# Performance work log

Measured on AMD Instinct MI355X. Metric: run time of the kernel, lower is better.

The kernel has to match this reference:

```python
import jax, jax.numpy as jnp
import numpy as np

TAU = 2.0        # spikingjelly LIFNode default tau
VTH = 1.0        # v_threshold
ALPHA = 2.0      # ATan surrogate alpha
NUM_HEADS = 8
N_WIN = 8
TOPK = 4


@jax.custom_vjp
def atan_heaviside(x):
    # spike = H(v - v_th), with ATan surrogate gradient
    return (x >= 0.0).astype(x.dtype)

def _ah_fwd(x):
    return atan_heaviside(x), x

def _ah_bwd(x, g):
    half_pi_alpha = np.float32(np.pi / 2.0 * ALPHA)
    return (g * (ALPHA / 2.0) / (1.0 + (half_pi_alpha * x) ** 2),)

atan_heaviside.defvjp(_ah_fwd, _ah_bwd)


def lif(x):
    """Multi-step LIF over leading time dim. decay_input=True, v_reset=0, detach_reset."""
    def step(v, xt):
        v = v + (xt - v) / TAU                      # charge
        s = atan_heaviside(v - VTH)                 # fire
        v = v * (1.0 - jax.lax.stop_gradient(s))    # hard reset (detached)
        return v, s
    _, spikes = jax.lax.scan(step, jnp.zeros_like(x[0]), x)
    return spikes


def setup_inputs() -> dict:
    key = jax.random.key(0)
    k1, k2, k3, k4, k5 = jax.random.split(key, 5)
    T, B, L, C = 4, 4, 1024, 256
    x = jax.random.normal(k1, (T, B, L, C), dtype=jnp.float32)
    w_qkv = jax.random.normal(k2, (C, 3 * C), dtype=jnp.float32) * (C ** -0.5)
    b_qkv = jax.random.normal(k3, (3 * C,), dtype=jnp.float32) * 0.02
    w_proj = jax.random.normal(k4, (C, C), dtype=jnp.float32) * (C ** -0.5)
    b_proj = jax.random.normal(k5, (C,), dtype=jnp.float32) * 0.02
    return {"x": x, "w_qkv": w_qkv, "b_qkv": b_qkv, "w_proj": w_proj, "b_proj": b_proj}


def reference(x, w_qkv, b_qkv, w_proj, b_proj):
    T, B, L, C = x.shape
    hd = C // NUM_HEADS
    win = L // N_WIN
    scale = hd ** -0.5

    # --- region-level routing (on raw input summed over time) ---
    xs = x.sum(axis=0).reshape(B, N_WIN, win, C)
    region = xs.sum(axis=2)                                  # [B, n_win, C]
    attn_r = jnp.einsum('bnc,bmc->bnm', region, region) * (C ** -0.5)
    _, idx = jax.lax.top_k(attn_r, TOPK)                     # [B, n_win, topk] int32

    # --- qkv + LIF spiking ---
    qkv = x @ w_qkv + b_qkv                                  # [T,B,L,3C]
    q, k, v = jnp.split(qkv, 3, axis=-1)
    q, k, v = lif(q), lif(k), lif(v)
    q = q.reshape(T, B, N_WIN, win, NUM_HEADS, hd)
    k = k.reshape(T, B, N_WIN, win, NUM_HEADS, hd)
    v = v.reshape(T, B, N_WIN, win, NUM_HEADS, hd)

    # --- gather routed KV windows (vectorized; topk-major concat like torch.cat) ---
    b_idx = jnp.arange(B)[:, None, None]                     # [B,1,1]
    k_g = k[:, b_idx, idx].reshape(T, B, N_WIN, TOPK * win, NUM_HEADS, hd)
    v_g = v[:, b_idx, idx].reshape(T, B, N_WIN, TOPK * win, NUM_HEADS, hd)

    # --- windowed attention over gathered keys ---
    attn = jnp.einsum('tbnqhd,tbnkhd->tbnhqk', q, k_g) * scale
    attn = jax.nn.softmax(attn, axis=-1)
    out = jnp.einsum('tbnhqk,tbnkhd->tbnqhd', attn, v_g).reshape(T, B, L, C)

    out = lif(out @ w_proj + b_proj)
    return out
```

## Files before the change

### kernel.cpp

```cpp
#include <hip/hip_runtime.h>
#include <cstdint>
#include <cstddef>

#define TT 4
#define BB 4
#define LL 1024
#define CC 256
#define HH 8
#define HD 32
#define NWIN 8
#define WIN 128
#define TOPKN 4
#define C3 768

__global__ __launch_bounds__(64) void region_kernel(const float* __restrict__ x,
                                                    float* __restrict__ region) {
    int bn = blockIdx.x;
    int b = bn >> 3, n = bn & 7;
    int c = blockIdx.y * 64 + threadIdx.x;
    float tot = 0.0f;
    for (int r = 0; r < WIN; ++r) {
        int l = n * WIN + r;
        float s = 0.0f;
        for (int t = 0; t < TT; ++t) {
            s += x[(((size_t)t * BB + b) * LL + l) * CC + c];
        }
        tot += s;
    }
    region[(size_t)bn * CC + c] = tot;
}

__global__ __launch_bounds__(64) void route_kernel(const float* __restrict__ region,
                                                   int* __restrict__ idx) {
    int b = blockIdx.x;
    __shared__ float reg[NWIN][CC];
    __shared__ float attn_r[NWIN][NWIN];
    int tid = threadIdx.x;
    for (int e = tid; e < NWIN * CC; e += 64)
        reg[e >> 8][e & 255] = region[(size_t)b * NWIN * CC + e];
    __syncthreads();
    int n = tid >> 3, m = tid & 7;
    float s = 0.0f;
    for (int c = 0; c < CC; ++c) s += reg[n][c] * reg[m][c];
    attn_r[n][m] = s * 0.0625f;
    __syncthreads();
    if (tid < NWIN) {
        float vals[NWIN];
        for (int m2 = 0; m2 < NWIN; ++m2) vals[m2] = attn_r[tid][m2];
        for (int kk = 0; kk < TOPKN; ++kk) {
            int bi = 0; float bv = vals[0];
            for (int m2 = 1; m2 < NWIN; ++m2) {
                if (vals[m2] > bv) { bv = vals[m2]; bi = m2; }
            }
            idx[(b * NWIN + tid) * TOPKN + kk] = bi;
            vals[bi] = -INFINITY;
        }
    }
}

__global__ __launch_bounds__(256, 3) void gemm_bias128(const float* __restrict__ A,
                                                       const float* __restrict__ W,
                                                       const float* __restrict__ bias,
                                                       float* __restrict__ C,
                                                       int M, int N, int K) {
    const int BM = 128, BN = 128, BK = 16, TM = 8;
    __shared__ float As[BK][BM + 4];
    __shared__ float Bs[BK][136];
    int tid = threadIdx.x;
    int tx = tid & 15, ty = tid >> 4;
    int bm = blockIdx.x * BM, bn = blockIdx.y * BN;
    float acc[TM][8] = {};
    for (int k0 = 0; k0 < K; k0 += BK) {
#pragma unroll
        for (int it = 0; it < 2; ++it) {
            int i = it * 256 + tid;
            int row = i >> 2, kc = (i & 3) * 4;
            float4 v = *(const float4*)(A + (size_t)(bm + row) * K + k0 + kc);
            As[kc + 0][row] = v.x; As[kc + 1][row] = v.y;
            As[kc + 2][row] = v.z; As[kc + 3][row] = v.w;
        }
#pragma unroll
        for (int it = 0; it < 2; ++it) {
            int i = it * 256 + tid;
            int kr = i >> 5, nc = (i & 31) * 4;
            float4 v = *(const float4*)(W + (size_t)(k0 + kr) * N + bn + nc);
            *(float4*)&Bs[kr][nc] = v;
        }
        __syncthreads();
#pragma unroll
        for (int kk = 0; kk < BK; ++kk) {
            float a[TM], bb[8];
            const float4* ap = (const float4*)&As[kk][ty * TM];
            float4 a0 = ap[0], a1 = ap[1];
            a[0]=a0.x; a[1]=a0.y; a[2]=a0.z; a[3]=a0.w;
            a[4]=a1.x; a[5]=a1.y; a[6]=a1.z; a[7]=a1.w;
            float4 b0 = *(const float4*)&Bs[kk][tx * 4];
            float4 b1 = *(const float4*)&Bs[kk][64 + tx * 4];
            bb[0]=b0.x; bb[1]=b0.y; bb[2]=b0.z; bb[3]=b0.w;
            bb[4]=b1.x; bb[5]=b1.y; bb[6]=b1.z; bb[7]=b1.w;
#pragma unroll
            for (int i = 0; i < TM; ++i)
#pragma unroll
                for (int j = 0; j < 8; ++j)
                    acc[i][j] = fmaf(a[i], bb[j], acc[i][j]);
        }
        __syncthreads();
    }
#pragma unroll
    for (int i = 0; i < TM; ++i) {
        int row = bm + ty * TM + i;
        int col0 = bn + tx * 4;
        int col1 = bn + 64 + tx * 4;
        float4 o0 = make_float4(acc[i][0] + bias[col0 + 0], acc[i][1] + bias[col0 + 1],
                                acc[i][2] + bias[col0 + 2], acc[i][3] + bias[col0 + 3]);
        float4 o1 = make_float4(acc[i][4] + bias[col1 + 0], acc[i][5] + bias[col1 + 1],
                                acc[i][6] + bias[col1 + 2], acc[i][7] + bias[col1 + 3]);
        *(float4*)&C[(size_t)row * N + col0] = o0;
        *(float4*)&C[(size_t)row * N + col1] = o1;
    }
}

__global__ __launch_bounds__(256, 4) void gemm_bias64(const float* __restrict__ A,
                                                      const float* __restrict__ W,
                                                      const float* __restrict__ bias,
                                                      float* __restrict__ C,
                                                      int M, int N, int K) {
    const int BM = 64, BN = 64, BK = 16;
    __shared__ float As[BK][BM + 4];
    __shared__ float Bs[BK][72];
    int tid = threadIdx.x;
    int tx = tid & 15, ty = tid >> 4;
    int bm = blockIdx.x * BM, bn = blockIdx.y * BN;
    float acc[4][4] = {};
    for (int k0 = 0; k0 < K; k0 += BK) {
        {
            int row = tid >> 2, kc = (tid & 3) * 4;
            float4 v = *(const float4*)(A + (size_t)(bm + row) * K + k0 + kc);
            As[kc + 0][row] = v.x; As[kc + 1][row] = v.y;
            As[kc + 2][row] = v.z; As[kc + 3][row] = v.w;
        }
        {
            int kr = tid >> 4, nc = (tid & 15) * 4;
            float4 v = *(const float4*)(W + (size_t)(k0 + kr) * N + bn + nc);
            *(float4*)&Bs[kr][nc] = v;
        }
        __syncthreads();
#pragma unroll
        for (int kk = 0; kk < BK; ++kk) {
            float4 av = *(const float4*)&As[kk][ty * 4];
            float4 bv = *(const float4*)&Bs[kk][tx * 4];
            float a[4] = {av.x, av.y, av.z, av.w};
            float bb[4] = {bv.x, bv.y, bv.z, bv.w};
#pragma unroll
            for (int i = 0; i < 4; ++i)
#pragma unroll
                for (int j = 0; j < 4; ++j)
                    acc[i][j] = fmaf(a[i], bb[j], acc[i][j]);
        }
        __syncthreads();
    }
#pragma unroll
    for (int i = 0; i < 4; ++i) {
        int row = bm + ty * 4 + i;
        int col = bn + tx * 4;
        float4 o = make_float4(acc[i][0] + bias[col + 0], acc[i][1] + bias[col + 1],
                               acc[i][2] + bias[col + 2], acc[i][3] + bias[col + 3]);
        *(float4*)&C[(size_t)row * N + col] = o;
    }
}

__global__ __launch_bounds__(256) void lif_kernel(const float* src, float* dst, size_t stride) {
    size_t i = ((size_t)blockIdx.x * blockDim.x + threadIdx.x) * 4;
    float v[4] = {0.f, 0.f, 0.f, 0.f};
    for (int t = 0; t < TT; ++t) {
        float4 xv4 = *(const float4*)(src + (size_t)t * stride + i);
        float xv[4] = {xv4.x, xv4.y, xv4.z, xv4.w};
        float sp[4];
#pragma unroll
        for (int j = 0; j < 4; ++j) {
            v[j] = v[j] + (xv[j] - v[j]) * 0.5f;
            bool fire = (v[j] >= 1.0f);
            sp[j] = fire ? 1.0f : 0.0f;
            v[j] = fire ? 0.0f : v[j];
        }
        *(float4*)(dst + (size_t)t * stride + i) = make_float4(sp[0], sp[1], sp[2], sp[3]);
    }
}

__global__ __launch_bounds__(192) void lif_pack_kernel(float* __restrict__ qkv,
                                                       uint32_t* __restrict__ pk) {
    int row = blockIdx.x;
    int tid = threadIdx.x;
    int c = tid * 4;
    int wid = tid >> 6;
    int lane = tid & 63;
    const size_t stride = (size_t)BB * LL * C3;
    float* base = qkv + (size_t)row * C3 + c;

    float v[4] = {0.f, 0.f, 0.f, 0.f};
    for (int t = 0; t < TT; ++t) {
        float4 xv4 = *(const float4*)(base + (size_t)t * stride);
        float xv[4] = {xv4.x, xv4.y, xv4.z, xv4.w};
        bool fire[4];
        float sp[4];
#pragma unroll
        for (int j = 0; j < 4; ++j) {
            v[j] = v[j] + (xv[j] - v[j]) * 0.5f;
            fire[j] = (v[j] >= 1.0f);
            sp[j] = fire[j] ? 1.0f : 0.0f;
            v[j] = fire[j] ? 0.0f : v[j];
        }
        if (c >= 512)
            *(float4*)(base + (size_t)t * stride) = make_float4(sp[0], sp[1], sp[2], sp[3]);
        unsigned long long B0 = __ballot(fire[0]);
        unsigned long long B1 = __ballot(fire[1]);
        unsigned long long B2 = __ballot(fire[2]);
        unsigned long long B3 = __ballot(fire[3]);
        if (lane < 8 && wid < 2) {
            uint32_t word = ((uint32_t)(B0 >> (8 * lane)) & 0xFFu)
                          | (((uint32_t)(B1 >> (8 * lane)) & 0xFFu) << 8)
                          | (((uint32_t)(B2 >> (8 * lane)) & 0xFFu) << 16)
                          | (((uint32_t)(B3 >> (8 * lane)) & 0xFFu) << 24);
            pk[((size_t)t * BB * LL + row) * 16 + wid * 8 + lane] = word;
        }
    }
}

__global__ __launch_bounds__(256, 4) void attn_pv(const float* __restrict__ spk,
                                                  const uint32_t* __restrict__ pk,
                                                  const int* __restrict__ idxws,
                                                  float* __restrict__ out) {
    int bid = blockIdx.x;
    int h = bid & 1, hp = (bid >> 1) & 3, n = (bid >> 3) & 7, b = (bid >> 6) & 3, t = bid >> 8;
    __shared__ __align__(16) float Vlds[2][64][32];
    __shared__ float ptab[33][WIN];
    __shared__ __align__(16) uint32_t kbs[4 * WIN];
    int tid = threadIdx.x;
    int qg = tid & 63, dh = tid >> 6;
    int lbase = (t * BB + b) * LL;

    const int* ip = idxws + (b * NWIN + n) * TOPKN;
    int s0r = ip[0], s1r = ip[1], s2r = ip[2], s3r = ip[3];

#pragma unroll 2
    for (int e = tid; e < 512; e += 256) {
        int w = e >> 7;
        int sw = (w == 0) ? s0r : (w == 1) ? s1r : (w == 2) ? s2r : s3r;
        int row = sw * WIN + (e & 127);
        kbs[e] = pk[(size_t)(lbase + row) * 16 + 8 + hp * 2 + h];
    }
    uint32_t qw0 = pk[(size_t)(lbase + n * WIN + qg) * 16 + hp * 2 + h];
    uint32_t qw1 = pk[(size_t)(lbase + n * WIN + qg + 64) * 16 + hp * 2 + h];

    const float* vsrc = spk + (size_t)lbase * C3 + 512 + hp * 64 + h * 32
                        + (size_t)(tid >> 3) * C3 + (tid & 7) * 4;
    int wvoff = (tid >> 6) * 1024;

#define STAGE_HALF(hw_)                                                              \
    do {                                                                             \
        int hw = (hw_);                                                              \
        int ww = hw >> 1;                                                            \
        int sw = (ww == 0) ? s0r : (ww == 1) ? s1r : (ww == 2) ? s2r : s3r;          \
        const float* src = vsrc + (size_t)sw * (WIN * C3)                            \
                                + (size_t)(hw & 1) * 64 * C3;                        \
        char* lb = (char*)(&Vlds[hw & 1][0][0]) + wvoff;                             \
        __builtin_amdgcn_global_load_lds(                                            \
            (const __attribute__((address_space(1))) void*)src,                      \
            (__attribute__((address_space(3))) void*)lb, 16, 0, 0);                  \
        __builtin_amdgcn_global_load_lds(                                            \
            (const __attribute__((address_space(1))) void*)(src + 32 * C3),          \
            (__attribute__((address_space(3))) void*)(lb + 4096), 16, 0, 0);         \
    } while (0)

    STAGE_HALF(0);
    STAGE_HALF(1);

    asm volatile("s_waitcnt lgkmcnt(0)" ::: "memory");
    __builtin_amdgcn_s_barrier();

    const float ALPHA_SC = 0.17677669529663687f;
    const uint4* kb4 = (const uint4*)kbs;
    if (tid < 128) {
        uint32_t qwt = (tid & 64) ? qw1 : qw0;
        int smax = 0;
#pragma unroll 8
        for (int k4 = 0; k4 < 128; ++k4) {
            uint4 w4 = kb4[k4];
            smax = max(smax, __popc(qwt & w4.x));
            smax = max(smax, __popc(qwt & w4.y));
            smax = max(smax, __popc(qwt & w4.z));
            smax = max(smax, __popc(qwt & w4.w));
        }
        float am = __fmul_rn((float)smax, ALPHA_SC);
        for (int s = 0; s <= 32; ++s)
            ptab[s][tid] = expf(__fsub_rn(__fmul_rn((float)s, ALPHA_SC), am));
        float Z = 0.0f;
#pragma unroll 4
        for (int k4 = 0; k4 < 128; ++k4) {
            uint4 w4 = kb4[k4];
            Z += ptab[__popc(qwt & w4.x)][tid];
            Z += ptab[__popc(qwt & w4.y)][tid];
            Z += ptab[__popc(qwt & w4.z)][tid];
            Z += ptab[__popc(qwt & w4.w)][tid];
        }
        for (int s = 0; s <= 32; ++s)
            ptab[s][tid] = ptab[s][tid] / Z;
    }

    float acc0[8], acc1[8];
#pragma unroll
    for (int d = 0; d < 8; ++d) { acc0[d] = 0.0f; acc1[d] = 0.0f; }

    asm volatile("s_waitcnt lgkmcnt(0)" ::: "memory");
    asm volatile("s_waitcnt vmcnt(2)" ::: "memory");
    __builtin_amdgcn_s_barrier();

#pragma unroll
    for (int hw = 0; hw < 8; ++hw) {
        const uint4* kw4 = kb4 + hw * 16;
        const float* vb = &Vlds[hw & 1][0][dh * 8];
#pragma unroll 2
        for (int g = 0; g < 16; ++g) {
            uint4 kw = kw4[g];
            const float* pr = vb + g * 128;
#pragma unroll
            for (int jp = 0; jp < 2; ++jp) {
                uint32_t ka = (jp == 0) ? kw.x : kw.z;
                uint32_t kb_ = (jp == 0) ? kw.y : kw.w;
                float Pa0 = ptab[__popc(qw0 & ka)][qg];
                float Pa1 = ptab[__popc(qw1 & ka)][qg + 64];
                float Pb0 = ptab[__popc(qw0 & kb_)][qg];
                float Pb1 = ptab[__popc(qw1 & kb_)][qg + 64];
                const float4* va = (const float4*)(pr + jp * 64);
                const float4* vbp = (const float4*)(pr + jp * 64 + 32);
                float4 a0 = va[0], a1 = va[1];
                float4 b0 = vbp[0], b1 = vbp[1];
                acc0[0] = fmaf(Pa0, a0.x, acc0[0]);  acc1[0] = fmaf(Pa1, a0.x, acc1[0]);
                acc0[1] = fmaf(Pa0, a0.y, acc0[1]);  acc1[1] = fmaf(Pa1, a0.y, acc1[1]);
                acc0[2] = fmaf(Pa0, a0.z, acc0[2]);  acc1[2] = fmaf(Pa1, a0.z, acc1[2]);
                acc0[3] = fmaf(Pa0, a0.w, acc0[3]);  acc1[3] = fmaf(Pa1, a0.w, acc1[3]);
                acc0[4] = fmaf(Pa0, a1.x, acc0[4]);  acc1[4] = fmaf(Pa1, a1.x, acc1[4]);
                acc0[5] = fmaf(Pa0, a1.y, acc0[5]);  acc1[5] = fmaf(Pa1, a1.y, acc1[5]);
                acc0[6] = fmaf(Pa0, a1.z, acc0[6]);  acc1[6] = fmaf(Pa1, a1.z, acc1[6]);
                acc0[7] = fmaf(Pa0, a1.w, acc0[7]);  acc1[7] = fmaf(Pa1, a1.w, acc1[7]);
                acc0[0] = fmaf(Pb0, b0.x, acc0[0]);  acc1[0] = fmaf(Pb1, b0.x, acc1[0]);
                acc0[1] = fmaf(Pb0, b0.y, acc0[1]);  acc1[1] = fmaf(Pb1, b0.y, acc1[1]);
                acc0[2] = fmaf(Pb0, b0.z, acc0[2]);  acc1[2] = fmaf(Pb1, b0.z, acc1[2]);
                acc0[3] = fmaf(Pb0, b0.w, acc0[3]);  acc1[3] = fmaf(Pb1, b0.w, acc1[3]);
                acc0[4] = fmaf(Pb0, b1.x, acc0[4]);  acc1[4] = fmaf(Pb1, b1.x, acc1[4]);
                acc0[5] = fmaf(Pb0, b1.y, acc0[5]);  acc1[5] = fmaf(Pb1, b1.y, acc1[5]);
                acc0[6] = fmaf(Pb0, b1.z, acc0[6]);  acc1[6] = fmaf(Pb1, b1.z, acc1[6]);
                acc0[7] = fmaf(Pb0, b1.w, acc0[7]);  acc1[7] = fmaf(Pb1, b1.w, acc1[7]);
            }
        }

        if (hw < 7) {
            __builtin_amdgcn_s_barrier();
            if (hw < 6) {
                STAGE_HALF(hw + 2);
                asm volatile("s_waitcnt vmcnt(2)" ::: "memory");
            } else {
                asm volatile("s_waitcnt vmcnt(0)" ::: "memory");
            }
            __builtin_amdgcn_s_barrier();
        }
    }
#undef STAGE_HALF

    size_t ob0 = (size_t)(lbase + n * WIN + qg) * CC + (hp * 2 + h) * 32 + dh * 8;
    size_t ob1 = ob0 + (size_t)64 * CC;
    *(float4*)&out[ob0]     = make_float4(acc0[0], acc0[1], acc0[2], acc0[3]);
    *(float4*)&out[ob0 + 4] = make_float4(acc0[4], acc0[5], acc0[6], acc0[7]);
    *(float4*)&out[ob1]     = make_float4(acc1[0], acc1[1], acc1[2], acc1[3]);
    *(float4*)&out[ob1 + 4] = make_float4(acc1[4], acc1[5], acc1[6], acc1[7]);
}

extern "C" void kernel_launch(void* const* d_in, const int* in_sizes, int n_in,
                              void* d_out, int out_size, void* d_ws, size_t ws_size,
                              hipStream_t stream) {
    const float* x      = (const float*)d_in[0];
    const float* w_qkv  = (const float*)d_in[1];
    const float* b_qkv  = (const float*)d_in[2];
    const float* w_proj = (const float*)d_in[3];
    const float* b_proj = (const float*)d_in[4];
    float* ws = (float*)d_ws;

    float* qkv      = ws;
    float* attn_out = ws + 12582912;
    float* proj     = ws + 16777216;
    uint32_t* pkb   = (uint32_t*)proj;
    float* region   = ws + 20971520;
    int*   idxp     = (int*)(ws + 20979712);
    float* outp     = (float*)d_out;

    region_kernel<<<dim3(BB * NWIN, 4), dim3(64), 0, stream>>>(x, region);
    route_kernel<<<dim3(BB), dim3(64), 0, stream>>>(region, idxp);
    gemm_bias128<<<dim3(128, 6), dim3(256), 0, stream>>>(x, w_qkv, b_qkv, qkv,
                                                         TT * BB * LL, C3, CC);
    lif_pack_kernel<<<dim3(BB * LL), dim3(192), 0, stream>>>(qkv, pkb);
    attn_pv<<<dim3(TT * BB * NWIN * 4 * 2), dim3(256), 0, stream>>>(qkv, pkb, idxp, attn_out);
    gemm_bias64<<<dim3(256, 4), dim3(256), 0, stream>>>(attn_out, w_proj, b_proj, proj,
                                                        TT * BB * LL, CC, CC);
    lif_kernel<<<dim3(1024), dim3(256), 0, stream>>>(proj, outp, (size_t)BB * LL * CC);
}
```

Measured before the change: 245.9 us.

## Merge head pair into one attn_pv block with 8 queries per thread

The attention-PV kernel now processes both heads of a head pair in a single 128-thread block instead of two 256-thread blocks. Each thread accumulates 8 query rows by 8 output dims, so every V value loaded from LDS is reused across 8 queries instead of 2. The V tile staged through LDS widens to 64 columns to cover both heads. Doubling the work per thread in this way aims to cut LDS traffic per FMA and the redundant staging of V. In exchange the grid is halved to 1024 blocks of 128 threads, register pressure rises (64 accumulators), and the main loop is no longer unrolled, which may reduce occupancy and latency hiding.

```diff
diff --git a/kernel.cpp b/kernel.cpp
--- a/kernel.cpp
+++ b/kernel.cpp
@@ -226,34 +226,37 @@
     }
 }
 
-__global__ __launch_bounds__(256, 4) void attn_pv(const float* __restrict__ spk,
+__global__ __launch_bounds__(128, 2) void attn_pv(const float* __restrict__ spk,
                                                   const uint32_t* __restrict__ pk,
                                                   const int* __restrict__ idxws,
                                                   float* __restrict__ out) {
     int bid = blockIdx.x;
-    int h = bid & 1, hp = (bid >> 1) & 3, n = (bid >> 3) & 7, b = (bid >> 6) & 3, t = bid >> 8;
-    __shared__ __align__(16) float Vlds[2][64][32];
-    __shared__ float ptab[33][WIN];
-    __shared__ __align__(16) uint32_t kbs[4 * WIN];
+    int hp = bid & 3, n = (bid >> 2) & 7, b = (bid >> 5) & 3, t = bid >> 7;
+    __shared__ __align__(16) float Vlds[2][64][64];
+    __shared__ float ptab[33][256];
+    __shared__ __align__(16) uint32_t kbs[2 * 512];
     int tid = threadIdx.x;
-    int qg = tid & 63, dh = tid >> 6;
+    int qg = tid & 15, dh = (tid >> 4) & 3, h = tid >> 6;
     int lbase = (t * BB + b) * LL;
 
     const int* ip = idxws + (b * NWIN + n) * TOPKN;
     int s0r = ip[0], s1r = ip[1], s2r = ip[2], s3r = ip[3];
 
-#pragma unroll 2
-    for (int e = tid; e < 512; e += 256) {
-        int w = e >> 7;
+#pragma unroll 8
+    for (int e = tid; e < 1024; e += 128) {
+        int hh = e >> 9, kk = e & 511;
+        int w = kk >> 7;
         int sw = (w == 0) ? s0r : (w == 1) ? s1r : (w == 2) ? s2r : s3r;
-        int row = sw * WIN + (e & 127);
-        kbs[e] = pk[(size_t)(lbase + row) * 16 + 8 + hp * 2 + h];
-    }
-    uint32_t qw0 = pk[(size_t)(lbase + n * WIN + qg) * 16 + hp * 2 + h];
-    uint32_t qw1 = pk[(size_t)(lbase + n * WIN + qg + 64) * 16 + hp * 2 + h];
-
-    const float* vsrc = spk + (size_t)lbase * C3 + 512 + hp * 64 + h * 32
-                        + (size_t)(tid >> 3) * C3 + (tid & 7) * 4;
+        int row = sw * WIN + (kk & 127);
+        kbs[e] = pk[(size_t)(lbase + row) * 16 + 8 + hp * 2 + hh];
+    }
+    uint32_t qw[8];
+#pragma unroll
+    for (int j = 0; j < 8; ++j)
+        qw[j] = pk[(size_t)(lbase + n * WIN + qg + 16 * j) * 16 + hp * 2 + h];
+
+    const float* vsrc = spk + (size_t)lbase * C3 + 512 + hp * 64
+                        + (size_t)(tid >> 4) * C3 + (tid & 15) * 4;
     int wvoff = (tid >> 6) * 1024;
 
 #define STAGE_HALF(hw_)                                                              \
@@ -261,15 +264,14 @@
         int hw = (hw_);                                                              \
         int ww = hw >> 1;                                                            \
         int sw = (ww == 0) ? s0r : (ww == 1) ? s1r : (ww == 2) ? s2r : s3r;          \
-        const float* src = vsrc + (size_t)sw * (WIN * C3)                            \
-                                + (size_t)(hw & 1) * 64 * C3;                        \
+        const float* src = vsrc + (size_t)(sw * WIN + (hw & 1) * 64) * C3;           \
         char* lb = (char*)(&Vlds[hw & 1][0][0]) + wvoff;                             \
-        __builtin_amdgcn_global_load_lds(                                            \
-            (const __attribute__((address_space(1))) void*)src,                      \
-            (__attribute__((address_space(3))) void*)lb, 16, 0, 0);                  \
-        __builtin_amdgcn_global_load_lds(                                            \
-            (const __attribute__((address_space(1))) void*)(src + 32 * C3),          \
-            (__attribute__((address_space(3))) void*)(lb + 4096), 16, 0, 0);         \
+        _Pragma("unroll")                                                            \
+        for (int it = 0; it < 8; ++it) {                                             \
+            __builtin_amdgcn_global_load_lds(                                        \
+                (const __attribute__((address_space(1))) void*)(src + (size_t)it * 8 * C3), \
+                (__attribute__((address_space(3))) void*)(lb + it * 2048), 16, 0, 0);\
+        }                                                                            \
     } while (0)
 
     STAGE_HALF(0);
@@ -279,13 +281,14 @@
     __builtin_amdgcn_s_barrier();
 
     const float ALPHA_SC = 0.17677669529663687f;
-    const uint4* kb4 = (const uint4*)kbs;
-    if (tid < 128) {
-        uint32_t qwt = (tid & 64) ? qw1 : qw0;
+    for (int u = tid; u < 256; u += 128) {
+        int qq = u & 127, hu = u >> 7;
+        uint32_t qwt = pk[(size_t)(lbase + n * WIN + qq) * 16 + hp * 2 + hu];
+        const uint4* kb4u = (const uint4*)(kbs + hu * 512);
         int smax = 0;
 #pragma unroll 8
         for (int k4 = 0; k4 < 128; ++k4) {
-            uint4 w4 = kb4[k4];
+            uint4 w4 = kb4u[k4];
             smax = max(smax, __popc(qwt & w4.x));
             smax = max(smax, __popc(qwt & w4.y));
             smax = max(smax, __popc(qwt & w4.z));
@@ -293,64 +296,67 @@
         }
         float am = __fmul_rn((float)smax, ALPHA_SC);
         for (int s = 0; s <= 32; ++s)
-            ptab[s][tid] = expf(__fsub_rn(__fmul_rn((float)s, ALPHA_SC), am));
+            ptab[s][u] = expf(__fsub_rn(__fmul_rn((float)s, ALPHA_SC), am));
         float Z = 0.0f;
 #pragma unroll 4
         for (int k4 = 0; k4 < 128; ++k4) {
-            uint4 w4 = kb4[k4];
-            Z += ptab[__popc(qwt & w4.x)][tid];
-            Z += ptab[__popc(qwt & w4.y)][tid];
-            Z += ptab[__popc(qwt & w4.z)][tid];
-            Z += ptab[__popc(qwt & w4.w)][tid];
+            uint4 w4 = kb4u[k4];
+            Z += ptab[__popc(qwt & w4.x)][u];
+            Z += ptab[__popc(qwt & w4.y)][u];
+            Z += ptab[__popc(qwt & w4.z)][u];
+            Z += ptab[__popc(qwt & w4.w)][u];
         }
         for (int s = 0; s <= 32; ++s)
-            ptab[s][tid] = ptab[s][tid] / Z;
-    }
-
-    float acc0[8], acc1[8];
-#pragma unroll
-    for (int d = 0; d < 8; ++d) { acc0[d] = 0.0f; acc1[d] = 0.0f; }
+            ptab[s][u] = ptab[s][u] / Z;
+    }
+
+    float acc[8][8];
+#pragma unroll
+    for (int j = 0; j < 8; ++j)
+#pragma unroll
+        for (int d = 0; d < 8; ++d) acc[j][d] = 0.0f;
 
     asm volatile("s_waitcnt lgkmcnt(0)" ::: "memory");
-    asm volatile("s_waitcnt vmcnt(2)" ::: "memory");
+    asm volatile("s_waitcnt vmcnt(8)" ::: "memory");
     __builtin_amdgcn_s_barrier();
 
-#pragma unroll
+    const uint4* kb4h = (const uint4*)(kbs + h * 512);
+    int hcol = h * 128 + qg;
+
+#pragma unroll 1
     for (int hw = 0; hw < 8; ++hw) {
-        const uint4* kw4 = kb4 + hw * 16;
-        const float* vb = &Vlds[hw & 1][0][dh * 8];
+        const uint4* kw4 = kb4h + hw * 16;
+        const float* vhalf = &Vlds[hw & 1][0][h * 32 + dh * 8];
 #pragma unroll 2
         for (int g = 0; g < 16; ++g) {
             uint4 kw = kw4[g];
-            const float* pr = vb + g * 128;
-#pragma unroll
-            for (int jp = 0; jp < 2; ++jp) {
-                uint32_t ka = (jp == 0) ? kw.x : kw.z;
-                uint32_t kb_ = (jp == 0) ? kw.y : kw.w;
-                float Pa0 = ptab[__popc(qw0 & ka)][qg];
-                float Pa1 = ptab[__popc(qw1 & ka)][qg + 64];
-                float Pb0 = ptab[__popc(qw0 & kb_)][qg];
-                float Pb1 = ptab[__popc(qw1 & kb_)][qg + 64];
-                const float4* va = (const float4*)(pr + jp * 64);
-                const float4* vbp = (const float4*)(pr + jp * 64 + 32);
-                float4 a0 = va[0], a1 = va[1];
-                float4 b0 = vbp[0], b1 = vbp[1];
-                acc0[0] = fmaf(Pa0, a0.x, acc0[0]);  acc1[0] = fmaf(Pa1, a0.x, acc1[0]);
-                acc0[1] = fmaf(Pa0, a0.y, acc0[1]);  acc1[1] = fmaf(Pa1, a0.y, acc1[1]);
-                acc0[2] = fmaf(Pa0, a0.z, acc0[2]);  acc1[2] = fmaf(Pa1, a0.z, acc1[2]);
-                acc0[3] = fmaf(Pa0, a0.w, acc0[3]);  acc1[3] = fmaf(Pa1, a0.w, acc1[3]);
-                acc0[4] = fmaf(Pa0, a1.x, acc0[4]);  acc1[4] = fmaf(Pa1, a1.x, acc1[4]);
-                acc0[5] = fmaf(Pa0, a1.y, acc0[5]);  acc1[5] = fmaf(Pa1, a1.y, acc1[5]);
-                acc0[6] = fmaf(Pa0, a1.z, acc0[6]);  acc1[6] = fmaf(Pa1, a1.z, acc1[6]);
-                acc0[7] = fmaf(Pa0, a1.w, acc0[7]);  acc1[7] = fmaf(Pa1, a1.w, acc1[7]);
-                acc0[0] = fmaf(Pb0, b0.x, acc0[0]);  acc1[0] = fmaf(Pb1, b0.x, acc1[0]);
-                acc0[1] = fmaf(Pb0, b0.y, acc0[1]);  acc1[1] = fmaf(Pb1, b0.y, acc1[1]);
-                acc0[2] = fmaf(Pb0, b0.z, acc0[2]);  acc1[2] = fmaf(Pb1, b0.z, acc1[2]);
-                acc0[3] = fmaf(Pb0, b0.w, acc0[3]);  acc1[3] = fmaf(Pb1, b0.w, acc1[3]);
-                acc0[4] = fmaf(Pb0, b1.x, acc0[4]);  acc1[4] = fmaf(Pb1, b1.x, acc1[4]);
-                acc0[5] = fmaf(Pb0, b1.y, acc0[5]);  acc1[5] = fmaf(Pb1, b1.y, acc1[5]);
-                acc0[6] = fmaf(Pb0, b1.z, acc0[6]);  acc1[6] = fmaf(Pb1, b1.z, acc1[6]);
-                acc0[7] = fmaf(Pb0, b1.w, acc0[7]);  acc1[7] = fmaf(Pb1, b1.w, acc1[7]);
+            const float* pr = vhalf + g * 256;
+#pragma unroll
+            for (int rr = 0; rr < 4; ++rr) {
+                uint32_t krow = (rr == 0) ? kw.x : (rr == 1) ? kw.y
+                              : (rr == 2) ? kw.z : kw.w;
+                float P0 = ptab[__popc(qw[0] & krow)][hcol];
+                float P1 = ptab[__popc(qw[1] & krow)][hcol + 16];
+                float P2 = ptab[__popc(qw[2] & krow)][hcol + 32];
+                float P3 = ptab[__popc(qw[3] & krow)][hcol + 48];
+                float P4 = ptab[__popc(qw[4] & krow)][hcol + 64];
+                float P5 = ptab[__popc(qw[5] & krow)][hcol + 80];
+                float P6 = ptab[__popc(qw[6] & krow)][hcol + 96];
+                float P7 = ptab[__popc(qw[7] & krow)][hcol + 112];
+                const float4* vp = (const float4*)(pr + rr * 64);
+                float4 v0 = vp[0], v1 = vp[1];
+                float vv[8] = {v0.x, v0.y, v0.z, v0.w, v1.x, v1.y, v1.z, v1.w};
+#pragma unroll
+                for (int d = 0; d < 8; ++d) {
+                    acc[0][d] = fmaf(P0, vv[d], acc[0][d]);
+                    acc[1][d] = fmaf(P1, vv[d], acc[1][d]);
+                    acc[2][d] = fmaf(P2, vv[d], acc[2][d]);
+                    acc[3][d] = fmaf(P3, vv[d], acc[3][d]);
+                    acc[4][d] = fmaf(P4, vv[d], acc[4][d]);
+                    acc[5][d] = fmaf(P5, vv[d], acc[5][d]);
+                    acc[6][d] = fmaf(P6, vv[d], acc[6][d]);
+                    acc[7][d] = fmaf(P7, vv[d], acc[7][d]);
+                }
             }
         }
 
@@ -358,7 +364,7 @@
             __builtin_amdgcn_s_barrier();
             if (hw < 6) {
                 STAGE_HALF(hw + 2);
-                asm volatile("s_waitcnt vmcnt(2)" ::: "memory");
+                asm volatile("s_waitcnt vmcnt(8)" ::: "memory");
             } else {
                 asm volatile("s_waitcnt vmcnt(0)" ::: "memory");
             }
@@ -367,12 +373,13 @@
     }
 #undef STAGE_HALF
 
-    size_t ob0 = (size_t)(lbase + n * WIN + qg) * CC + (hp * 2 + h) * 32 + dh * 8;
-    size_t ob1 = ob0 + (size_t)64 * CC;
-    *(float4*)&out[ob0]     = make_float4(acc0[0], acc0[1], acc0[2], acc0[3]);
-    *(float4*)&out[ob0 + 4] = make_float4(acc0[4], acc0[5], acc0[6], acc0[7]);
-    *(float4*)&out[ob1]     = make_float4(acc1[0], acc1[1], acc1[2], acc1[3]);
-    *(float4*)&out[ob1 + 4] = make_float4(acc1[4], acc1[5], acc1[6], acc1[7]);
+#pragma unroll
+    for (int j = 0; j < 8; ++j) {
+        size_t ob = (size_t)(lbase + n * WIN + qg + 16 * j) * CC
+                    + (hp * 2 + h) * 32 + dh * 8;
+        *(float4*)&out[ob]     = make_float4(acc[j][0], acc[j][1], acc[j][2], acc[j][3]);
+        *(float4*)&out[ob + 4] = make_float4(acc[j][4], acc[j][5], acc[j][6], acc[j][7]);
+    }
 }
 
 extern "C" void kernel_launch(void* const* d_in, const int* in_sizes, int n_in,
@@ -398,7 +405,7 @@
     gemm_bias128<<<dim3(128, 6), dim3(256), 0, stream>>>(x, w_qkv, b_qkv, qkv,
                                                          TT * BB * LL, C3, CC);
     lif_pack_kernel<<<dim3(BB * LL), dim3(192), 0, stream>>>(qkv, pkb);
-    attn_pv<<<dim3(TT * BB * NWIN * 4 * 2), dim3(256), 0, stream>>>(qkv, pkb, idxp, attn_out);
+    attn_pv<<<dim3(TT * BB * NWIN * 4), dim3(128), 0, stream>>>(qkv, pkb, idxp, attn_out);
     gemm_bias64<<<dim3(256, 4), dim3(256), 0, stream>>>(attn_out, w_proj, b_proj, proj,
                                                         TT * BB * LL, CC, CC);
     lif_kernel<<<dim3(1024), dim3(256), 0, stream>>>(proj, outp, (size_t)BB * LL * CC);
```

Measured after the change: 258.1 us. 1.05x slower.

## Halve attn_pv block size and give each thread four query rows

Applied to the files above, without the earlier changes.

The attention kernel now runs 128 threads per block instead of 256. Each thread accumulates four query rows over an 8-wide head-dim slice, so every V value loaded from LDS is reused across four rows. All 128 threads now share the softmax-table build, where previously half the block sat idle. V staging issues four LDS-direct loads per thread instead of two, the wait counts are adjusted to match, and the hw loop is no longer unrolled. In exchange it uses more accumulator registers and has fewer waves per block to hide LDS and memory latency.

```diff
diff --git a/kernel.cpp b/kernel.cpp
--- a/kernel.cpp
+++ b/kernel.cpp
@@ -226,7 +226,7 @@
     }
 }
 
-__global__ __launch_bounds__(256, 4) void attn_pv(const float* __restrict__ spk,
+__global__ __launch_bounds__(128, 2) void attn_pv(const float* __restrict__ spk,
                                                   const uint32_t* __restrict__ pk,
                                                   const int* __restrict__ idxws,
                                                   float* __restrict__ out) {
@@ -234,23 +234,24 @@
     int h = bid & 1, hp = (bid >> 1) & 3, n = (bid >> 3) & 7, b = (bid >> 6) & 3, t = bid >> 8;
     __shared__ __align__(16) float Vlds[2][64][32];
     __shared__ float ptab[33][WIN];
-    __shared__ __align__(16) uint32_t kbs[4 * WIN];
-    int tid = threadIdx.x;
-    int qg = tid & 63, dh = tid >> 6;
+    __shared__ __align__(16) uint32_t kbs[512];
+    int tid = threadIdx.x;
+    int qg = tid & 31, dh = tid >> 5;
     int lbase = (t * BB + b) * LL;
 
     const int* ip = idxws + (b * NWIN + n) * TOPKN;
     int s0r = ip[0], s1r = ip[1], s2r = ip[2], s3r = ip[3];
 
-#pragma unroll 2
-    for (int e = tid; e < 512; e += 256) {
+#pragma unroll 4
+    for (int e = tid; e < 512; e += 128) {
         int w = e >> 7;
         int sw = (w == 0) ? s0r : (w == 1) ? s1r : (w == 2) ? s2r : s3r;
-        int row = sw * WIN + (e & 127);
-        kbs[e] = pk[(size_t)(lbase + row) * 16 + 8 + hp * 2 + h];
-    }
-    uint32_t qw0 = pk[(size_t)(lbase + n * WIN + qg) * 16 + hp * 2 + h];
-    uint32_t qw1 = pk[(size_t)(lbase + n * WIN + qg + 64) * 16 + hp * 2 + h];
+        kbs[e] = pk[(size_t)(lbase + sw * WIN + (e & 127)) * 16 + 8 + hp * 2 + h];
+    }
+    uint32_t qw[4];
+#pragma unroll
+    for (int j = 0; j < 4; ++j)
+        qw[j] = pk[(size_t)(lbase + n * WIN + qg + 32 * j) * 16 + hp * 2 + h];
 
     const float* vsrc = spk + (size_t)lbase * C3 + 512 + hp * 64 + h * 32
                         + (size_t)(tid >> 3) * C3 + (tid & 7) * 4;
@@ -261,15 +262,14 @@
         int hw = (hw_);                                                              \
         int ww = hw >> 1;                                                            \
         int sw = (ww == 0) ? s0r : (ww == 1) ? s1r : (ww == 2) ? s2r : s3r;          \
-        const float* src = vsrc + (size_t)sw * (WIN * C3)                            \
-                                + (size_t)(hw & 1) * 64 * C3;                        \
+        const float* src = vsrc + (size_t)(sw * WIN + (hw & 1) * 64) * C3;           \
         char* lb = (char*)(&Vlds[hw & 1][0][0]) + wvoff;                             \
-        __builtin_amdgcn_global_load_lds(                                            \
-            (const __attribute__((address_space(1))) void*)src,                      \
-            (__attribute__((address_space(3))) void*)lb, 16, 0, 0);                  \
-        __builtin_amdgcn_global_load_lds(                                            \
-            (const __attribute__((address_space(1))) void*)(src + 32 * C3),          \
-            (__attribute__((address_space(3))) void*)(lb + 4096), 16, 0, 0);         \
+        _Pragma("unroll")                                                            \
+        for (int it = 0; it < 4; ++it) {                                             \
+            __builtin_amdgcn_global_load_lds(                                        \
+                (const __attribute__((address_space(1))) void*)(src + (size_t)it * 16 * C3), \
+                (__attribute__((address_space(3))) void*)(lb + it * 2048), 16, 0, 0);\
+        }                                                                            \
     } while (0)
 
     STAGE_HALF(0);
@@ -280,8 +280,8 @@
 
     const float ALPHA_SC = 0.17677669529663687f;
     const uint4* kb4 = (const uint4*)kbs;
-    if (tid < 128) {
-        uint32_t qwt = (tid & 64) ? qw1 : qw0;
+    {
+        uint32_t qwt = qw[dh];
         int smax = 0;
 #pragma unroll 8
         for (int k4 = 0; k4 < 128; ++k4) {
@@ -307,15 +307,17 @@
             ptab[s][tid] = ptab[s][tid] / Z;
     }
 
-    float acc0[8], acc1[8];
-#pragma unroll
-    for (int d = 0; d < 8; ++d) { acc0[d] = 0.0f; acc1[d] = 0.0f; }
+    float acc[4][8];
+#pragma unroll
+    for (int j = 0; j < 4; ++j)
+#pragma unroll
+        for (int e = 0; e < 8; ++e) acc[j][e] = 0.0f;
 
     asm volatile("s_waitcnt lgkmcnt(0)" ::: "memory");
-    asm volatile("s_waitcnt vmcnt(2)" ::: "memory");
+    asm volatile("s_waitcnt vmcnt(4)" ::: "memory");
     __builtin_amdgcn_s_barrier();
 
-#pragma unroll
+#pragma unroll 1
     for (int hw = 0; hw < 8; ++hw) {
         const uint4* kw4 = kb4 + hw * 16;
         const float* vb = &Vlds[hw & 1][0][dh * 8];
@@ -324,33 +326,23 @@
             uint4 kw = kw4[g];
             const float* pr = vb + g * 128;
 #pragma unroll
-            for (int jp = 0; jp < 2; ++jp) {
-                uint32_t ka = (jp == 0) ? kw.x : kw.z;
-                uint32_t kb_ = (jp == 0) ? kw.y : kw.w;
-                float Pa0 = ptab[__popc(qw0 & ka)][qg];
-                float Pa1 = ptab[__popc(qw1 & ka)][qg + 64];
-                float Pb0 = ptab[__popc(qw0 & kb_)][qg];
-                float Pb1 = ptab[__popc(qw1 & kb_)][qg + 64];
-                const float4* va = (const float4*)(pr + jp * 64);
-                const float4* vbp = (const float4*)(pr + jp * 64 + 32);
-                float4 a0 = va[0], a1 = va[1];
-                float4 b0 = vbp[0], b1 = vbp[1];
-                acc0[0] = fmaf(Pa0, a0.x, acc0[0]);  acc1[0] = fmaf(Pa1, a0.x, acc1[0]);
-                acc0[1] = fmaf(Pa0, a0.y, acc0[1]);  acc1[1] = fmaf(Pa1, a0.y, acc1[1]);
-                acc0[2] = fmaf(Pa0, a0.z, acc0[2]);  acc1[2] = fmaf(Pa1, a0.z, acc1[2]);
-                acc0[3] = fmaf(Pa0, a0.w, acc0[3]);  acc1[3] = fmaf(Pa1, a0.w, acc1[3]);
-                acc0[4] = fmaf(Pa0, a1.x, acc0[4]);  acc1[4] = fmaf(Pa1, a1.x, acc1[4]);
-                acc0[5] = fmaf(Pa0, a1.y, acc0[5]);  acc1[5] = fmaf(Pa1, a1.y, acc1[5]);
-                acc0[6] = fmaf(Pa0, a1.z, acc0[6]);  acc1[6] = fmaf(Pa1, a1.z, acc1[6]);
-                acc0[7] = fmaf(Pa0, a1.w, acc0[7]);  acc1[7] = fmaf(Pa1, a1.w, acc1[7]);
-                acc0[0] = fmaf(Pb0, b0.x, acc0[0]);  acc1[0] = fmaf(Pb1, b0.x, acc1[0]);
-                acc0[1] = fmaf(Pb0, b0.y, acc0[1]);  acc1[1] = fmaf(Pb1, b0.y, acc1[1]);
-                acc0[2] = fmaf(Pb0, b0.z, acc0[2]);  acc1[2] = fmaf(Pb1, b0.z, acc1[2]);
-                acc0[3] = fmaf(Pb0, b0.w, acc0[3]);  acc1[3] = fmaf(Pb1, b0.w, acc1[3]);
-                acc0[4] = fmaf(Pb0, b1.x, acc0[4]);  acc1[4] = fmaf(Pb1, b1.x, acc1[4]);
-                acc0[5] = fmaf(Pb0, b1.y, acc0[5]);  acc1[5] = fmaf(Pb1, b1.y, acc1[5]);
-                acc0[6] = fmaf(Pb0, b1.z, acc0[6]);  acc1[6] = fmaf(Pb1, b1.z, acc1[6]);
-                acc0[7] = fmaf(Pb0, b1.w, acc0[7]);  acc1[7] = fmaf(Pb1, b1.w, acc1[7]);
+            for (int r = 0; r < 4; ++r) {
+                uint32_t krow = (r == 0) ? kw.x : (r == 1) ? kw.y
+                              : (r == 2) ? kw.z : kw.w;
+                float P0 = ptab[__popc(qw[0] & krow)][qg];
+                float P1 = ptab[__popc(qw[1] & krow)][qg + 32];
+                float P2 = ptab[__popc(qw[2] & krow)][qg + 64];
+                float P3 = ptab[__popc(qw[3] & krow)][qg + 96];
+                const float4* vp = (const float4*)(pr + r * 32);
+                float4 v0 = vp[0], v1 = vp[1];
+                float vv[8] = {v0.x, v0.y, v0.z, v0.w, v1.x, v1.y, v1.z, v1.w};
+#pragma unroll
+                for (int e = 0; e < 8; ++e) {
+                    acc[0][e] = fmaf(P0, vv[e], acc[0][e]);
+                    acc[1][e] = fmaf(P1, vv[e], acc[1][e]);
+                    acc[2][e] = fmaf(P2, vv[e], acc[2][e]);
+                    acc[3][e] = fmaf(P3, vv[e], acc[3][e]);
+                }
             }
         }
 
@@ -358,7 +350,7 @@
             __builtin_amdgcn_s_barrier();
             if (hw < 6) {
                 STAGE_HALF(hw + 2);
-                asm volatile("s_waitcnt vmcnt(2)" ::: "memory");
+                asm volatile("s_waitcnt vmcnt(4)" ::: "memory");
             } else {
                 asm volatile("s_waitcnt vmcnt(0)" ::: "memory");
             }
@@ -367,12 +359,13 @@
     }
 #undef STAGE_HALF
 
-    size_t ob0 = (size_t)(lbase + n * WIN + qg) * CC + (hp * 2 + h) * 32 + dh * 8;
-    size_t ob1 = ob0 + (size_t)64 * CC;
-    *(float4*)&out[ob0]     = make_float4(acc0[0], acc0[1], acc0[2], acc0[3]);
-    *(float4*)&out[ob0 + 4] = make_float4(acc0[4], acc0[5], acc0[6], acc0[7]);
-    *(float4*)&out[ob1]     = make_float4(acc1[0], acc1[1], acc1[2], acc1[3]);
-    *(float4*)&out[ob1 + 4] = make_float4(acc1[4], acc1[5], acc1[6], acc1[7]);
+#pragma unroll
+    for (int j = 0; j < 4; ++j) {
+        size_t ob = (size_t)(lbase + n * WIN + qg + 32 * j) * CC
+                    + (hp * 2 + h) * 32 + dh * 8;
+        *(float4*)&out[ob]     = make_float4(acc[j][0], acc[j][1], acc[j][2], acc[j][3]);
+        *(float4*)&out[ob + 4] = make_float4(acc[j][4], acc[j][5], acc[j][6], acc[j][7]);
+    }
 }
 
 extern "C" void kernel_launch(void* const* d_in, const int* in_sizes, int n_in,
@@ -398,7 +391,7 @@
     gemm_bias128<<<dim3(128, 6), dim3(256), 0, stream>>>(x, w_qkv, b_qkv, qkv,
                                                          TT * BB * LL, C3, CC);
     lif_pack_kernel<<<dim3(BB * LL), dim3(192), 0, stream>>>(qkv, pkb);
-    attn_pv<<<dim3(TT * BB * NWIN * 4 * 2), dim3(256), 0, stream>>>(qkv, pkb, idxp, attn_out);
+    attn_pv<<<dim3(TT * BB * NWIN * 4 * 2), dim3(128), 0, stream>>>(qkv, pkb, idxp, attn_out);
     gemm_bias64<<<dim3(256, 4), dim3(256), 0, stream>>>(attn_out, w_proj, b_proj, proj,
                                                         TT * BB * LL, CC, CC);
     lif_kernel<<<dim3(1024), dim3(256), 0, stream>>>(proj, outp, (size_t)BB * LL * CC);
```

Measured after the change: 243.4 us. About the same (-1.0%).
